# Kernel tuning notes

Hardware: AMD Instinct MI355X
Metric: run time of the kernel (lower is better)

The kernel has to match this reference:

```python
import jax, jax.numpy as jnp
import numpy as np

B, S, E, H, D = 4, 1024, 192, 64, 3  # head_dim pinned to 3 by the rotation matmul


def setup_inputs() -> dict:
    key = jax.random.key(0)
    k = jax.random.split(key, 6)
    x = jax.random.normal(k[0], (B, S, E), dtype=jnp.float32)
    w_scale = 1.0 / np.sqrt(E).astype(np.float32)
    Wq = jax.random.uniform(k[1], (E, E), jnp.float32, -w_scale, w_scale)
    Wk = jax.random.uniform(k[2], (E, E), jnp.float32, -w_scale, w_scale)
    Wv = jax.random.uniform(k[3], (E, E), jnp.float32, -w_scale, w_scale)
    Wo = jax.random.uniform(k[4], (E, E), jnp.float32, -w_scale, w_scale)
    rot = jax.random.normal(k[5], (H, D, D), dtype=jnp.float32)  # (num_heads, head_dim, 3), head_dim==3
    return {"x": x, "Wq": Wq, "Wk": Wk, "Wv": Wv, "Wo": Wo, "rot": rot}


def reference(x, Wq, Wk, Wv, Wo, rot):
    b, s, e = x.shape
    h, d, _ = rot.shape
    # projections (torch Linear: y = x @ W.T), split heads -> (b, h, s, d)
    q = jnp.einsum('bse,oe->bso', x, Wq).reshape(b, s, h, d).swapaxes(1, 2)
    k = jnp.einsum('bse,oe->bso', x, Wk).reshape(b, s, h, d).swapaxes(1, 2)
    v = jnp.einsum('bse,oe->bso', x, Wv).reshape(b, s, h, d).swapaxes(1, 2)
    # per-head learnable rotation folded into q and k
    q = jnp.einsum('bhsd,hde->bhse', q, rot)
    k = jnp.einsum('bhsd,hde->bhse', k, rot)
    scores = jnp.einsum('bhqd,bhkd->bhqk', q, k) / jnp.sqrt(jnp.asarray(d, x.dtype))
    attn = jax.nn.softmax(scores, axis=-1)
    out = jnp.einsum('bhqk,bhkd->bhqd', attn, v)  # (b, h, s, d)
    out = out.swapaxes(1, 2).reshape(b, s, e)
    return jnp.einsum('bse,oe->bso', out, Wo)
```

## Files before the change

kernel.cpp:

```cpp
#include <hip/hip_runtime.h>
#include <hip/hip_bf16.h>

#define BB 4
#define SS 1024
#define EE 192
#define HH 64

constexpr int BH = BB * HH;

typedef __attribute__((ext_vector_type(8))) short bs8;
typedef __attribute__((ext_vector_type(16))) float fx16;
union U4B { uint4 u; bs8 s; };

constexpr size_t OFF_WQR = 0;
constexpr size_t OFF_WKR = OFF_WQR + (size_t)EE*EE;
constexpr size_t OFF_Q   = OFF_WKR + (size_t)EE*EE;
constexpr size_t OFF_KF  = OFF_Q  + (size_t)BH*SS*4;
constexpr size_t OFF_VC  = OFF_KF + (size_t)BH*SS*2;
constexpr size_t OFF_AO  = OFF_VC + (size_t)BH*SS*3/2;

static __device__ __forceinline__ float fast_exp2(float x) {
#if __has_builtin(__builtin_amdgcn_exp2f)
  return __builtin_amdgcn_exp2f(x);
#else
  return exp2f(x);
#endif
}
static __device__ __forceinline__ float fast_rcp(float x) {
#if __has_builtin(__builtin_amdgcn_rcpf)
  return __builtin_amdgcn_rcpf(x);
#else
  return 1.0f / x;
#endif
}

__global__ __launch_bounds__(256) void fold_rot_k(
    const float* __restrict__ Wq, const float* __restrict__ Wk,
    const float* __restrict__ rot, float* __restrict__ WqR, float* __restrict__ WkR)
{
  int t = blockIdx.x * 256 + threadIdx.x;
  if (t >= 2 * EE * EE) return;
  int mat = t / (EE * EE);
  int idx = t % (EE * EE);
  int op = idx / EE, e = idx % EE;
  int h = op / 3, ep = op - h * 3;
  const float* W = mat ? Wk : Wq;
  float acc = 0.f;
#pragma unroll
  for (int d = 0; d < 3; ++d)
    acc += rot[h * 9 + d * 3 + ep] * W[(h * 3 + d) * EE + e];
  float scale = mat ? 1.0f : 0.8329876360019913f;
  (mat ? WkR : WqR)[op * EE + e] = acc * scale;
}

__global__ __launch_bounds__(256) void gemm_qkv_k(
    const float* __restrict__ x, const float* __restrict__ WqR,
    const float* __restrict__ WkR, const float* __restrict__ Wv,
    float* __restrict__ Q, __hip_bfloat16* __restrict__ Kf, __hip_bfloat16* __restrict__ Vc)
{
  __shared__ __align__(16) float xs[64][68];
  __shared__ __align__(16) float wsm[64][68];
  int bx = blockIdx.x;
  int by = blockIdx.y;
  int t = threadIdx.x;
  int sel = bx / 3;
  const float* W = (sel == 0) ? WqR : (sel == 1 ? WkR : Wv);
  int colBase = (bx % 3) * 64;
  int rowBase = by * 64;
  int lrow = t >> 2, lq = t & 3;
  int tr = t & 15, tc = t >> 4;
  float acc[4][4] = {};

  for (int kk = 0; kk < 3; ++kk) {
    const float* xg = x + (size_t)(rowBase + lrow) * EE + kk * 64;
    const float* wg = W + (size_t)(colBase + lrow) * EE + kk * 64;
    float4 xv[4], wv[4];
#pragma unroll
    for (int i = 0; i < 4; ++i) {
      xv[i] = ((const float4*)xg)[lq + 4 * i];
      wv[i] = ((const float4*)wg)[lq + 4 * i];
    }
    __syncthreads();
#pragma unroll
    for (int i = 0; i < 4; ++i) {
      int k0 = (lq + 4 * i) * 4;
      xs[k0 + 0][lrow] = xv[i].x; xs[k0 + 1][lrow] = xv[i].y;
      xs[k0 + 2][lrow] = xv[i].z; xs[k0 + 3][lrow] = xv[i].w;
      wsm[k0 + 0][lrow] = wv[i].x; wsm[k0 + 1][lrow] = wv[i].y;
      wsm[k0 + 2][lrow] = wv[i].z; wsm[k0 + 3][lrow] = wv[i].w;
    }
    __syncthreads();
#pragma unroll 8
    for (int k = 0; k < 64; ++k) {
      float4 a = *(const float4*)&xs[k][tr * 4];
      float4 bv = *(const float4*)&wsm[k][tc * 4];
      acc[0][0] += a.x * bv.x; acc[0][1] += a.x * bv.y; acc[0][2] += a.x * bv.z; acc[0][3] += a.x * bv.w;
      acc[1][0] += a.y * bv.x; acc[1][1] += a.y * bv.y; acc[1][2] += a.y * bv.z; acc[1][3] += a.y * bv.w;
      acc[2][0] += a.z * bv.x; acc[2][1] += a.z * bv.y; acc[2][2] += a.z * bv.z; acc[2][3] += a.z * bv.w;
      acc[3][0] += a.w * bv.x; acc[3][1] += a.w * bv.y; acc[3][2] += a.w * bv.z; acc[3][3] += a.w * bv.w;
    }
  }

#pragma unroll
  for (int i = 0; i < 4; ++i) {
    int r = rowBase + tr * 4 + i;
    int b = r >> 10, s = r & (SS - 1);
#pragma unroll
    for (int j = 0; j < 4; ++j) {
      int o = colBase + tc * 4 + j;
      int h = o / 3, d = o - h * 3;
      size_t bh = (size_t)(b * HH + h);
      if (sel == 0) {
        Q[(bh * SS + s) * 4 + d] = acc[i][j];
      } else if (sel == 1) {
        Kf[(bh * SS + s) * 4 + d] = __float2bfloat16(acc[i][j]);
        if (d == 2) Kf[(bh * SS + s) * 4 + 3] = __float2bfloat16(0.0f);
      } else {
        Vc[bh * (3 * SS) + (size_t)d * SS + s] = __float2bfloat16(acc[i][j]);
      }
    }
  }
}

__global__ __launch_bounds__(256, 4) void attn_k(
    const float* __restrict__ Qw, const unsigned short* __restrict__ Kfg,
    const unsigned short* __restrict__ Vcg, float* __restrict__ AO)
{
  __shared__ __align__(16) short KfL[1024 * 4];
  __shared__ __align__(16) short VcL[4 * 1040];
  int bh = blockIdx.x & 255;
  int eighth = blockIdx.x >> 8;
  int b = bh >> 6, h = bh & 63;

  const uint2* ksrc = (const uint2*)Kfg + (size_t)bh * 1024;
  uint2* kdst = (uint2*)KfL;
  for (int i = threadIdx.x; i < 1024; i += 256) kdst[i] = ksrc[i];
  const uint4* vsrc = (const uint4*)Vcg + (size_t)bh * 384;
  for (int i = threadIdx.x; i < 384; i += 256) {
    int r = i >> 7, cq = i & 127;
    *(uint4*)(VcL + r * 1040 + cq * 8) = vsrc[i];
  }
  {
    unsigned v1 = 0x3F803F80u;
    for (int i = threadIdx.x; i < 128; i += 256)
      *(uint4*)(VcL + 3 * 1040 + i * 8) = make_uint4(v1, v1, v1, v1);
  }
  __syncthreads();

  int lane = threadIdx.x & 63, w = threadIdx.x >> 6;
  int h32 = lane >> 5;
  int col = lane & 31;
  int q32 = eighth * 128 + w * 32;

  float4 qv = *(const float4*)&Qw[((size_t)bh * SS + q32 + col) * 4];
  unsigned pa, pb;
  asm("v_cvt_pk_bf16_f32 %0, %1, %2" : "=v"(pa) : "v"(qv.x), "v"(qv.y));
  asm("v_cvt_pk_bf16_f32 %0, %1, %2" : "=v"(pb) : "v"(qv.z), "v"(0.0f));
  U4B bq; bq.u = make_uint4(h32 ? 0u : pa, h32 ? 0u : pb, 0u, 0u);

  const fx16 zc = {0,0,0,0, 0,0,0,0, 0,0,0,0, 0,0,0,0};
  fx16 accPV = zc;
  int vbase = (col & 3) * 1040 + 8 * h32;

  for (int kt = 0; kt < 32; ++kt) {
    uint2 kk = *(const uint2*)(KfL + (size_t)(kt * 32 + col) * 4);
    U4B ak; ak.u = make_uint4(kk.x, kk.y, 0u, 0u);
    U4B bv1; bv1.u = *(const uint4*)(VcL + vbase + kt * 32);
    U4B bv2; bv2.u = *(const uint4*)(VcL + vbase + kt * 32 + 16);

    fx16 S = __builtin_amdgcn_mfma_f32_32x32x16_bf16(ak.s, bq.s, zc, 0, 0, 0);
    asm("" : "+v"(S));
#pragma unroll
    for (int i = 0; i < 16; ++i) S[i] = fast_exp2(S[i]);
    unsigned u0, u1, u2, u3, u4, u5, u6, u7;
    asm("v_cvt_pk_bf16_f32 %0, %1, %2" : "=v"(u0) : "v"(S[0]),  "v"(S[1]));
    asm("v_cvt_pk_bf16_f32 %0, %1, %2" : "=v"(u1) : "v"(S[2]),  "v"(S[3]));
    asm("v_cvt_pk_bf16_f32 %0, %1, %2" : "=v"(u2) : "v"(S[4]),  "v"(S[5]));
    asm("v_cvt_pk_bf16_f32 %0, %1, %2" : "=v"(u3) : "v"(S[6]),  "v"(S[7]));
    asm("v_cvt_pk_bf16_f32 %0, %1, %2" : "=v"(u4) : "v"(S[8]),  "v"(S[9]));
    asm("v_cvt_pk_bf16_f32 %0, %1, %2" : "=v"(u5) : "v"(S[10]), "v"(S[11]));
    asm("v_cvt_pk_bf16_f32 %0, %1, %2" : "=v"(u6) : "v"(S[12]), "v"(S[13]));
    asm("v_cvt_pk_bf16_f32 %0, %1, %2" : "=v"(u7) : "v"(S[14]), "v"(S[15]));
    asm("v_permlane32_swap_b32 %0, %1" : "+v"(u0), "+v"(u2));
    asm("v_permlane32_swap_b32 %0, %1" : "+v"(u1), "+v"(u3));
    asm("v_permlane32_swap_b32 %0, %1" : "+v"(u4), "+v"(u6));
    asm("v_permlane32_swap_b32 %0, %1" : "+v"(u5), "+v"(u7));
    U4B p1; p1.u = make_uint4(u0, u1, u2, u3);
    U4B p2; p2.u = make_uint4(u4, u5, u6, u7);
    accPV = __builtin_amdgcn_mfma_f32_32x32x16_bf16(p1.s, bv1.s, accPV, 0, 0, 0);
    accPV = __builtin_amdgcn_mfma_f32_32x32x16_bf16(p2.s, bv2.s, accPV, 0, 0, 0);
  }

  int base3 = (lane & 32) | 3;
  float inv[16];
#pragma unroll
  for (int rg = 0; rg < 16; ++rg)
    inv[rg] = __shfl(fast_rcp(accPV[rg]), base3, 64);
  if (col < 3) {
#pragma unroll
    for (int rg = 0; rg < 16; ++rg) {
      int row = (rg & 3) + 8 * (rg >> 2) + 4 * h32;
      AO[((size_t)(b * SS + q32 + row)) * EE + h * 3 + col] = accPV[rg] * inv[rg];
    }
  }
}

__global__ __launch_bounds__(256) void gemm_out_k(
    const float* __restrict__ x, const float* __restrict__ Wo, float* __restrict__ out)
{
  __shared__ __align__(16) float xs[64][68];
  __shared__ __align__(16) float wsm[64][68];
  int bx = blockIdx.x;
  int by = blockIdx.y;
  int t = threadIdx.x;
  int colBase = bx * 64;
  int rowBase = by * 64;
  int lrow = t >> 2, lq = t & 3;
  int tr = t & 15, tc = t >> 4;
  float acc[4][4] = {};

  for (int kk = 0; kk < 3; ++kk) {
    const float* xg = x + (size_t)(rowBase + lrow) * EE + kk * 64;
    const float* wg = Wo + (size_t)(colBase + lrow) * EE + kk * 64;
    float4 xv[4], wv[4];
#pragma unroll
    for (int i = 0; i < 4; ++i) {
      xv[i] = ((const float4*)xg)[lq + 4 * i];
      wv[i] = ((const float4*)wg)[lq + 4 * i];
    }
    __syncthreads();
#pragma unroll
    for (int i = 0; i < 4; ++i) {
      int k0 = (lq + 4 * i) * 4;
      xs[k0 + 0][lrow] = xv[i].x; xs[k0 + 1][lrow] = xv[i].y;
      xs[k0 + 2][lrow] = xv[i].z; xs[k0 + 3][lrow] = xv[i].w;
      wsm[k0 + 0][lrow] = wv[i].x; wsm[k0 + 1][lrow] = wv[i].y;
      wsm[k0 + 2][lrow] = wv[i].z; wsm[k0 + 3][lrow] = wv[i].w;
    }
    __syncthreads();
#pragma unroll 8
    for (int k = 0; k < 64; ++k) {
      float4 a = *(const float4*)&xs[k][tr * 4];
      float4 bv = *(const float4*)&wsm[k][tc * 4];
      acc[0][0] += a.x * bv.x; acc[0][1] += a.x * bv.y; acc[0][2] += a.x * bv.z; acc[0][3] += a.x * bv.w;
      acc[1][0] += a.y * bv.x; acc[1][1] += a.y * bv.y; acc[1][2] += a.y * bv.z; acc[1][3] += a.y * bv.w;
      acc[2][0] += a.z * bv.x; acc[2][1] += a.z * bv.y; acc[2][2] += a.z * bv.z; acc[2][3] += a.z * bv.w;
      acc[3][0] += a.w * bv.x; acc[3][1] += a.w * bv.y; acc[3][2] += a.w * bv.z; acc[3][3] += a.w * bv.w;
    }
  }

#pragma unroll
  for (int i = 0; i < 4; ++i) {
    int r = rowBase + tr * 4 + i;
#pragma unroll
    for (int j = 0; j < 4; ++j) {
      int o = colBase + tc * 4 + j;
      out[(size_t)r * EE + o] = acc[i][j];
    }
  }
}

extern "C" void kernel_launch(void* const* d_in, const int* in_sizes, int n_in,
                              void* d_out, int out_size, void* d_ws, size_t ws_size,
                              hipStream_t stream) {
  const float* x   = (const float*)d_in[0];
  const float* Wq  = (const float*)d_in[1];
  const float* Wk  = (const float*)d_in[2];
  const float* Wv  = (const float*)d_in[3];
  const float* Wo  = (const float*)d_in[4];
  const float* rot = (const float*)d_in[5];
  float* ws  = (float*)d_ws;
  float* WqR = ws + OFF_WQR;
  float* WkR = ws + OFF_WKR;
  float* Q   = ws + OFF_Q;
  unsigned short* Kf = (unsigned short*)(ws + OFF_KF);
  unsigned short* Vc = (unsigned short*)(ws + OFF_VC);
  float* AO  = ws + OFF_AO;
  float* out = (float*)d_out;

  fold_rot_k<<<dim3((2 * EE * EE + 255) / 256), 256, 0, stream>>>(Wq, Wk, rot, WqR, WkR);
  gemm_qkv_k<<<dim3(9, 64), 256, 0, stream>>>(x, WqR, WkR, Wv, Q,
                                              (__hip_bfloat16*)Kf, (__hip_bfloat16*)Vc);
  attn_k<<<dim3(BH * 8), 256, 0, stream>>>(Q, Kf, Vc, AO);
  gemm_out_k<<<dim3(3, 64), 256, 0, stream>>>(AO, Wo, out);
}
```

Baseline: 77.38 us.

## Move QKV and output projections onto bf16x3 split MFMA

```diff
diff --git a/kernel.cpp b/kernel.cpp
--- a/kernel.cpp
+++ b/kernel.cpp
@@ -12,12 +12,14 @@
 typedef __attribute__((ext_vector_type(16))) float fx16;
 union U4B { uint4 u; bs8 s; };
 
-constexpr size_t OFF_WQR = 0;
-constexpr size_t OFF_WKR = OFF_WQR + (size_t)EE*EE;
-constexpr size_t OFF_Q   = OFF_WKR + (size_t)EE*EE;
+constexpr size_t OFF_Q   = 0;
 constexpr size_t OFF_KF  = OFF_Q  + (size_t)BH*SS*4;
 constexpr size_t OFF_VC  = OFF_KF + (size_t)BH*SS*2;
 constexpr size_t OFF_AO  = OFF_VC + (size_t)BH*SS*3/2;
+constexpr size_t OFF_WCH = OFF_AO + (size_t)BB*SS*EE;
+constexpr size_t OFF_WCL = OFF_WCH + (size_t)576*EE/2;
+constexpr size_t OFF_WOH = OFF_WCL + (size_t)576*EE/2;
+constexpr size_t OFF_WOL = OFF_WOH + (size_t)EE*EE/2;
 
 static __device__ __forceinline__ float fast_exp2(float x) {
 #if __has_builtin(__builtin_amdgcn_exp2f)
@@ -34,90 +36,127 @@
 #endif
 }
 
-__global__ __launch_bounds__(256) void fold_rot_k(
+static __device__ __forceinline__ void split2(float a, float b, unsigned& hi, unsigned& lo) {
+  unsigned h;
+  asm("v_cvt_pk_bf16_f32 %0, %1, %2" : "=v"(h) : "v"(a), "v"(b));
+  float ha = __uint_as_float(h << 16);
+  float hb = __uint_as_float(h & 0xFFFF0000u);
+  float la = a - ha, lb = b - hb;
+  unsigned l;
+  asm("v_cvt_pk_bf16_f32 %0, %1, %2" : "=v"(l) : "v"(la), "v"(lb));
+  hi = h; lo = l;
+}
+
+__global__ __launch_bounds__(256) void fold_split_k(
     const float* __restrict__ Wq, const float* __restrict__ Wk,
-    const float* __restrict__ rot, float* __restrict__ WqR, float* __restrict__ WkR)
+    const float* __restrict__ Wv, const float* __restrict__ Wo,
+    const float* __restrict__ rot,
+    __hip_bfloat16* __restrict__ Wch, __hip_bfloat16* __restrict__ Wcl,
+    __hip_bfloat16* __restrict__ Woh, __hip_bfloat16* __restrict__ Wol)
 {
   int t = blockIdx.x * 256 + threadIdx.x;
-  if (t >= 2 * EE * EE) return;
-  int mat = t / (EE * EE);
-  int idx = t % (EE * EE);
-  int op = idx / EE, e = idx % EE;
-  int h = op / 3, ep = op - h * 3;
-  const float* W = mat ? Wk : Wq;
-  float acc = 0.f;
-#pragma unroll
-  for (int d = 0; d < 3; ++d)
-    acc += rot[h * 9 + d * 3 + ep] * W[(h * 3 + d) * EE + e];
-  float scale = mat ? 1.0f : 0.8329876360019913f;
-  (mat ? WkR : WqR)[op * EE + e] = acc * scale;
+  float val;
+  __hip_bfloat16 *ph, *pl;
+  int idx;
+  if (t < 576 * EE) {
+    int o = t / EE, e = t - o * EE;
+    int s3 = o / 192, oo = o - s3 * 192;
+    int h = oo / 3, ep = oo - h * 3;
+    if (s3 == 2) {
+      val = Wv[(size_t)oo * EE + e];
+    } else {
+      const float* W = s3 ? Wk : Wq;
+      float acc = 0.f;
+#pragma unroll
+      for (int d = 0; d < 3; ++d)
+        acc += rot[h * 9 + d * 3 + ep] * W[(size_t)(h * 3 + d) * EE + e];
+      val = acc * (s3 ? 1.0f : 0.8329876360019913f);
+    }
+    ph = Wch; pl = Wcl; idx = t;
+  } else {
+    int u = t - 576 * EE;
+    if (u >= EE * EE) return;
+    val = Wo[u]; ph = Woh; pl = Wol; idx = u;
+  }
+  __hip_bfloat16 hi = __float2bfloat16(val);
+  float lo = val - __bfloat162float(hi);
+  ph[idx] = hi;
+  pl[idx] = __float2bfloat16(lo);
 }
 
 __global__ __launch_bounds__(256) void gemm_qkv_k(
-    const float* __restrict__ x, const float* __restrict__ WqR,
-    const float* __restrict__ WkR, const float* __restrict__ Wv,
+    const float* __restrict__ x,
+    const unsigned short* __restrict__ Wch, const unsigned short* __restrict__ Wcl,
     float* __restrict__ Q, __hip_bfloat16* __restrict__ Kf, __hip_bfloat16* __restrict__ Vc)
 {
-  __shared__ __align__(16) float xs[64][68];
-  __shared__ __align__(16) float wsm[64][68];
-  int bx = blockIdx.x;
-  int by = blockIdx.y;
+  __shared__ __align__(16) short xh[64][72], xl[64][72];
+  __shared__ __align__(16) short wh[64][72], wl[64][72];
+  int colBase = blockIdx.x * 64;
+  int rowBase = blockIdx.y * 64;
   int t = threadIdx.x;
-  int sel = bx / 3;
-  const float* W = (sel == 0) ? WqR : (sel == 1 ? WkR : Wv);
-  int colBase = (bx % 3) * 64;
-  int rowBase = by * 64;
-  int lrow = t >> 2, lq = t & 3;
-  int tr = t & 15, tc = t >> 4;
-  float acc[4][4] = {};
+  int lane = t & 63, w = t >> 6;
+  int wr = w >> 1, wc = w & 1;
+  int l31 = lane & 31, lh = lane >> 5;
+
+  const fx16 zc = {0,0,0,0, 0,0,0,0, 0,0,0,0, 0,0,0,0};
+  fx16 acc = zc;
+
+  int srow = t >> 2, sk = (t & 3) * 16;
 
   for (int kk = 0; kk < 3; ++kk) {
-    const float* xg = x + (size_t)(rowBase + lrow) * EE + kk * 64;
-    const float* wg = W + (size_t)(colBase + lrow) * EE + kk * 64;
-    float4 xv[4], wv[4];
-#pragma unroll
-    for (int i = 0; i < 4; ++i) {
-      xv[i] = ((const float4*)xg)[lq + 4 * i];
-      wv[i] = ((const float4*)wg)[lq + 4 * i];
-    }
+    const float4* xg = (const float4*)&x[(size_t)(rowBase + srow) * EE + kk * 64 + sk];
+    float4 v0 = xg[0], v1 = xg[1], v2 = xg[2], v3 = xg[3];
+    const uint4* whg = (const uint4*)&Wch[(size_t)(colBase + srow) * EE + kk * 64 + sk];
+    const uint4* wlg = (const uint4*)&Wcl[(size_t)(colBase + srow) * EE + kk * 64 + sk];
+    uint4 wh0 = whg[0], wh1 = whg[1], wl0 = wlg[0], wl1 = wlg[1];
+
+    unsigned hu[8], lu[8];
+    split2(v0.x, v0.y, hu[0], lu[0]); split2(v0.z, v0.w, hu[1], lu[1]);
+    split2(v1.x, v1.y, hu[2], lu[2]); split2(v1.z, v1.w, hu[3], lu[3]);
+    split2(v2.x, v2.y, hu[4], lu[4]); split2(v2.z, v2.w, hu[5], lu[5]);
+    split2(v3.x, v3.y, hu[6], lu[6]); split2(v3.z, v3.w, hu[7], lu[7]);
+
     __syncthreads();
-#pragma unroll
-    for (int i = 0; i < 4; ++i) {
-      int k0 = (lq + 4 * i) * 4;
-      xs[k0 + 0][lrow] = xv[i].x; xs[k0 + 1][lrow] = xv[i].y;
-      xs[k0 + 2][lrow] = xv[i].z; xs[k0 + 3][lrow] = xv[i].w;
-      wsm[k0 + 0][lrow] = wv[i].x; wsm[k0 + 1][lrow] = wv[i].y;
-      wsm[k0 + 2][lrow] = wv[i].z; wsm[k0 + 3][lrow] = wv[i].w;
-    }
+    *(uint4*)&xh[srow][sk]     = make_uint4(hu[0], hu[1], hu[2], hu[3]);
+    *(uint4*)&xh[srow][sk + 8] = make_uint4(hu[4], hu[5], hu[6], hu[7]);
+    *(uint4*)&xl[srow][sk]     = make_uint4(lu[0], lu[1], lu[2], lu[3]);
+    *(uint4*)&xl[srow][sk + 8] = make_uint4(lu[4], lu[5], lu[6], lu[7]);
+    *(uint4*)&wh[srow][sk]     = wh0;
+    *(uint4*)&wh[srow][sk + 8] = wh1;
+    *(uint4*)&wl[srow][sk]     = wl0;
+    *(uint4*)&wl[srow][sk + 8] = wl1;
     __syncthreads();
-#pragma unroll 8
-    for (int k = 0; k < 64; ++k) {
-      float4 a = *(const float4*)&xs[k][tr * 4];
-      float4 bv = *(const float4*)&wsm[k][tc * 4];
-      acc[0][0] += a.x * bv.x; acc[0][1] += a.x * bv.y; acc[0][2] += a.x * bv.z; acc[0][3] += a.x * bv.w;
-      acc[1][0] += a.y * bv.x; acc[1][1] += a.y * bv.y; acc[1][2] += a.y * bv.z; acc[1][3] += a.y * bv.w;
-      acc[2][0] += a.z * bv.x; acc[2][1] += a.z * bv.y; acc[2][2] += a.z * bv.z; acc[2][3] += a.z * bv.w;
-      acc[3][0] += a.w * bv.x; acc[3][1] += a.w * bv.y; acc[3][2] += a.w * bv.z; acc[3][3] += a.w * bv.w;
-    }
-  }
-
-#pragma unroll
-  for (int i = 0; i < 4; ++i) {
-    int r = rowBase + tr * 4 + i;
-    int b = r >> 10, s = r & (SS - 1);
-#pragma unroll
-    for (int j = 0; j < 4; ++j) {
-      int o = colBase + tc * 4 + j;
-      int h = o / 3, d = o - h * 3;
-      size_t bh = (size_t)(b * HH + h);
-      if (sel == 0) {
-        Q[(bh * SS + s) * 4 + d] = acc[i][j];
-      } else if (sel == 1) {
-        Kf[(bh * SS + s) * 4 + d] = __float2bfloat16(acc[i][j]);
-        if (d == 2) Kf[(bh * SS + s) * 4 + 3] = __float2bfloat16(0.0f);
-      } else {
-        Vc[bh * (3 * SS) + (size_t)d * SS + s] = __float2bfloat16(acc[i][j]);
-      }
+
+#pragma unroll
+    for (int ks = 0; ks < 4; ++ks) {
+      int ac = ks * 16 + lh * 8;
+      U4B Ah, Al, Bh, Bl;
+      Ah.u = *(const uint4*)&xh[wr * 32 + l31][ac];
+      Al.u = *(const uint4*)&xl[wr * 32 + l31][ac];
+      Bh.u = *(const uint4*)&wh[wc * 32 + l31][ac];
+      Bl.u = *(const uint4*)&wl[wc * 32 + l31][ac];
+      acc = __builtin_amdgcn_mfma_f32_32x32x16_bf16(Ah.s, Bh.s, acc, 0, 0, 0);
+      acc = __builtin_amdgcn_mfma_f32_32x32x16_bf16(Al.s, Bh.s, acc, 0, 0, 0);
+      acc = __builtin_amdgcn_mfma_f32_32x32x16_bf16(Ah.s, Bl.s, acc, 0, 0, 0);
+    }
+  }
+
+  int o = colBase + wc * 32 + l31;
+  int s3 = o / 192, oo = o - s3 * 192;
+  int hh = oo / 3, d = oo - hh * 3;
+#pragma unroll
+  for (int r = 0; r < 16; ++r) {
+    int row = rowBase + wr * 32 + (r & 3) + 8 * (r >> 2) + 4 * lh;
+    int b = row >> 10, s = row & (SS - 1);
+    size_t bh = (size_t)(b * HH + hh);
+    float v = acc[r];
+    if (s3 == 0) {
+      Q[(bh * SS + s) * 4 + d] = v;
+    } else if (s3 == 1) {
+      Kf[(bh * SS + s) * 4 + d] = __float2bfloat16(v);
+      if (d == 2) Kf[(bh * SS + s) * 4 + 3] = __float2bfloat16(0.0f);
+    } else {
+      Vc[bh * (3 * SS) + (size_t)d * SS + s] = __float2bfloat16(v);
     }
   }
 }
@@ -206,57 +245,67 @@
 }
 
 __global__ __launch_bounds__(256) void gemm_out_k(
-    const float* __restrict__ x, const float* __restrict__ Wo, float* __restrict__ out)
+    const float* __restrict__ AO,
+    const unsigned short* __restrict__ Woh, const unsigned short* __restrict__ Wol,
+    float* __restrict__ out)
 {
-  __shared__ __align__(16) float xs[64][68];
-  __shared__ __align__(16) float wsm[64][68];
-  int bx = blockIdx.x;
-  int by = blockIdx.y;
+  __shared__ __align__(16) short xh[64][72], xl[64][72];
+  __shared__ __align__(16) short wh[64][72], wl[64][72];
+  int colBase = blockIdx.x * 64;
+  int rowBase = blockIdx.y * 64;
   int t = threadIdx.x;
-  int colBase = bx * 64;
-  int rowBase = by * 64;
-  int lrow = t >> 2, lq = t & 3;
-  int tr = t & 15, tc = t >> 4;
-  float acc[4][4] = {};
+  int lane = t & 63, w = t >> 6;
+  int wr = w >> 1, wc = w & 1;
+  int l31 = lane & 31, lh = lane >> 5;
+
+  const fx16 zc = {0,0,0,0, 0,0,0,0, 0,0,0,0, 0,0,0,0};
+  fx16 acc = zc;
+
+  int srow = t >> 2, sk = (t & 3) * 16;
 
   for (int kk = 0; kk < 3; ++kk) {
-    const float* xg = x + (size_t)(rowBase + lrow) * EE + kk * 64;
-    const float* wg = Wo + (size_t)(colBase + lrow) * EE + kk * 64;
-    float4 xv[4], wv[4];
-#pragma unroll
-    for (int i = 0; i < 4; ++i) {
-      xv[i] = ((const float4*)xg)[lq + 4 * i];
-      wv[i] = ((const float4*)wg)[lq + 4 * i];
-    }
+    const float4* xg = (const float4*)&AO[(size_t)(rowBase + srow) * EE + kk * 64 + sk];
+    float4 v0 = xg[0], v1 = xg[1], v2 = xg[2], v3 = xg[3];
+    const uint4* whg = (const uint4*)&Woh[(size_t)(colBase + srow) * EE + kk * 64 + sk];
+    const uint4* wlg = (const uint4*)&Wol[(size_t)(colBase + srow) * EE + kk * 64 + sk];
+    uint4 wh0 = whg[0], wh1 = whg[1], wl0 = wlg[0], wl1 = wlg[1];
+
+    unsigned hu[8], lu[8];
+    split2(v0.x, v0.y, hu[0], lu[0]); split2(v0.z, v0.w, hu[1], lu[1]);
+    split2(v1.x, v1.y, hu[2], lu[2]); split2(v1.z, v1.w, hu[3], lu[3]);
+    split2(v2.x, v2.y, hu[4], lu[4]); split2(v2.z, v2.w, hu[5], lu[5]);
+    split2(v3.x, v3.y, hu[6], lu[6]); split2(v3.z, v3.w, hu[7], lu[7]);
+
     __syncthreads();
-#pragma unroll
-    for (int i = 0; i < 4; ++i) {
-      int k0 = (lq + 4 * i) * 4;
-      xs[k0 + 0][lrow] = xv[i].x; xs[k0 + 1][lrow] = xv[i].y;
-      xs[k0 + 2][lrow] = xv[i].z; xs[k0 + 3][lrow] = xv[i].w;
-      wsm[k0 + 0][lrow] = wv[i].x; wsm[k0 + 1][lrow] = wv[i].y;
-      wsm[k0 + 2][lrow] = wv[i].z; wsm[k0 + 3][lrow] = wv[i].w;
-    }
+    *(uint4*)&xh[srow][sk]     = make_uint4(hu[0], hu[1], hu[2], hu[3]);
+    *(uint4*)&xh[srow][sk + 8] = make_uint4(hu[4], hu[5], hu[6], hu[7]);
+    *(uint4*)&xl[srow][sk]     = make_uint4(lu[0], lu[1], lu[2], lu[3]);
+    *(uint4*)&xl[srow][sk + 8] = make_uint4(lu[4], lu[5], lu[6], lu[7]);
+    *(uint4*)&wh[srow][sk]     = wh0;
+    *(uint4*)&wh[srow][sk + 8] = wh1;
+    *(uint4*)&wl[srow][sk]     = wl0;
+    *(uint4*)&wl[srow][sk + 8] = wl1;
     __syncthreads();
-#pragma unroll 8
-    for (int k = 0; k < 64; ++k) {
-      float4 a = *(const float4*)&xs[k][tr * 4];
-      float4 bv = *(const float4*)&wsm[k][tc * 4];
-      acc[0][0] += a.x * bv.x; acc[0][1] += a.x * bv.y; acc[0][2] += a.x * bv.z; acc[0][3] += a.x * bv.w;
-      acc[1][0] += a.y * bv.x; acc[1][1] += a.y * bv.y; acc[1][2] += a.y * bv.z; acc[1][3] += a.y * bv.w;
-      acc[2][0] += a.z * bv.x; acc[2][1] += a.z * bv.y; acc[2][2] += a.z * bv.z; acc[2][3] += a.z * bv.w;
-      acc[3][0] += a.w * bv.x; acc[3][1] += a.w * bv.y; acc[3][2] += a.w * bv.z; acc[3][3] += a.w * bv.w;
-    }
-  }
-
-#pragma unroll
-  for (int i = 0; i < 4; ++i) {
-    int r = rowBase + tr * 4 + i;
-#pragma unroll
-    for (int j = 0; j < 4; ++j) {
-      int o = colBase + tc * 4 + j;
-      out[(size_t)r * EE + o] = acc[i][j];
-    }
+
+#pragma unroll
+    for (int ks = 0; ks < 4; ++ks) {
+      int ac = ks * 16 + lh * 8;
+      U4B Ah, Al, Bh, Bl;
+      Ah.u = *(const uint4*)&xh[wr * 32 + l31][ac];
+      Al.u = *(const uint4*)&xl[wr * 32 + l31][ac];
+      Bh.u = *(const uint4*)&wh[wc * 32 + l31][ac];
+      Bl.u = *(const uint4*)&wl[wc * 32 + l31][ac];
+      acc = __builtin_amdgcn_mfma_f32_32x32x16_bf16(Ah.s, Bh.s, acc, 0, 0, 0);
+      acc = __builtin_amdgcn_mfma_f32_32x32x16_bf16(Al.s, Bh.s, acc, 0, 0, 0);
+      acc = __builtin_amdgcn_mfma_f32_32x32x16_bf16(Ah.s, Bl.s, acc, 0, 0, 0);
+    }
+  }
+
+  int o = colBase + wc * 32 + l31;
+#pragma unroll
+  for (int r = 0; r < 16; ++r) {
+    int row = rowBase + wr * 32 + (r & 3) + 8 * (r >> 2) + 4 * lh;
+    out[(size_t)row * EE + o] = acc[r];
   }
 }
 
@@ -270,17 +319,22 @@
   const float* Wo  = (const float*)d_in[4];
   const float* rot = (const float*)d_in[5];
   float* ws  = (float*)d_ws;
-  float* WqR = ws + OFF_WQR;
-  float* WkR = ws + OFF_WKR;
   float* Q   = ws + OFF_Q;
-  unsigned short* Kf = (unsigned short*)(ws + OFF_KF);
-  unsigned short* Vc = (unsigned short*)(ws + OFF_VC);
+  unsigned short* Kf  = (unsigned short*)(ws + OFF_KF);
+  unsigned short* Vc  = (unsigned short*)(ws + OFF_VC);
   float* AO  = ws + OFF_AO;
+  unsigned short* Wch = (unsigned short*)(ws + OFF_WCH);
+  unsigned short* Wcl = (unsigned short*)(ws + OFF_WCL);
+  unsigned short* Woh = (unsigned short*)(ws + OFF_WOH);
+  unsigned short* Wol = (unsigned short*)(ws + OFF_WOL);
   float* out = (float*)d_out;
 
-  fold_rot_k<<<dim3((2 * EE * EE + 255) / 256), 256, 0, stream>>>(Wq, Wk, rot, WqR, WkR);
-  gemm_qkv_k<<<dim3(9, 64), 256, 0, stream>>>(x, WqR, WkR, Wv, Q,
+  fold_split_k<<<dim3((576 * EE + EE * EE) / 256), 256, 0, stream>>>(
+      Wq, Wk, Wv, Wo, rot,
+      (__hip_bfloat16*)Wch, (__hip_bfloat16*)Wcl,
+      (__hip_bfloat16*)Woh, (__hip_bfloat16*)Wol);
+  gemm_qkv_k<<<dim3(9, 64), 256, 0, stream>>>(x, Wch, Wcl, Q,
                                               (__hip_bfloat16*)Kf, (__hip_bfloat16*)Vc);
   attn_k<<<dim3(BH * 8), 256, 0, stream>>>(Q, Kf, Vc, AO);
-  gemm_out_k<<<dim3(3, 64), 256, 0, stream>>>(AO, Wo, out);
-}
+  gemm_out_k<<<dim3(3, 64), 256, 0, stream>>>(AO, Woh, Wol, out);
+}
```

Result: faster. 63.85 us (-17.5%).
